# Kernel optimization log

Measured on AMD Instinct MI355X. Metric: run time of the kernel, lower is better.

The kernel has to match this reference:

```python
import jax, jax.numpy as jnp
import numpy as np

SIGMA = 0.1

def setup_inputs() -> dict:
    key = jax.random.key(0)
    k1, k2, k3 = jax.random.split(key, 3)
    B = 16384
    risk_scores = jax.random.normal(k1, (B,), dtype=jnp.float32)
    times = jax.random.uniform(k2, (B,), dtype=jnp.float32)
    events = jax.random.randint(k3, (B,), 0, 2, dtype=jnp.int32)
    return {"risk_scores": risk_scores, "times": times, "events": events}

def reference(risk_scores, times, events):
    # mask[i, j] = (times[i] < times[j]) and (events[i] == 1)
    mask = (times[:, None] < times[None, :]) & (events[:, None] == 1)  # [B, B] bool
    maskf = mask.astype(risk_scores.dtype)
    # diff[i, j] = risk_scores[j] - risk_scores[i]
    diff = risk_scores[None, :] - risk_scores[:, None]  # [B, B]
    loss = jnp.sum(jax.nn.sigmoid(diff / SIGMA) * maskf)
    count = jnp.sum(maskf)
    return loss / (count + 1e-06)
```

## Files before the change

kernel.cpp:

```cpp
#include <hip/hip_runtime.h>


#define BLOCK 256
#define RPT 4
#define ROWS_PER_TILE (BLOCK * RPT)
#define JTILE 64
#define NCOLGRP 256
#define GRID_MAIN 2048

__device__ __forceinline__ float fast_exp2(float x) { return __builtin_amdgcn_exp2f(x); }
__device__ __forceinline__ float fast_rcp(float x)  { return __builtin_amdgcn_rcpf(x); }
__device__ __forceinline__ float clamp60(float x)   { return fminf(fmaxf(x, -60.0f), 60.0f); }

__global__ __launch_bounds__(BLOCK) void k_compact(
    const float* __restrict__ r, const float* __restrict__ t,
    const int* __restrict__ ev, int B, float kscale,
    int* __restrict__ cursor,
    float2* __restrict__ sI, float2* __restrict__ sJ) {
    int g = blockIdx.x * BLOCK + threadIdx.x;
    if (g >= B) return;
    float tv = t[g];
    float s  = clamp60(r[g] * kscale);
    sJ[g] = make_float2(fast_exp2(-s), tv);
    bool pred = (ev[g] == 1);
    unsigned long long m = __ballot(pred);
    int lane = threadIdx.x & 63;
    int before = __popcll(m & ((1ull << lane) - 1ull));
    int total = __popcll(m);
    int base = 0;
    if (lane == 0 && total > 0) base = atomicAdd(cursor, total);
    base = __shfl(base, 0);
    if (pred) sI[base + before] = make_float2(fast_exp2(s), tv);
}

__global__ __launch_bounds__(BLOCK) void k_main(
    const float2* __restrict__ sI, const float2* __restrict__ sJ,
    const int* __restrict__ nactive_g,
    float* __restrict__ pL, unsigned int* __restrict__ pC) {

    const int tid = threadIdx.x;
    const int nactive = *nactive_g;
    const int nrc = (nactive + ROWS_PER_TILE - 1) / ROWS_PER_TILE;
    const int ntiles = nrc * NCOLGRP;

    __shared__ float2 tile[JTILE];

    float lsum = 0.0f;
    int   csum = 0;

    for (int tix = blockIdx.x; tix < ntiles; tix += gridDim.x) {
        int rc = tix >> 8;
        int cg = tix & (NCOLGRP - 1);

        float E[RPT], T[RPT];
        int rbase = rc * ROWS_PER_TILE;
#pragma unroll
        for (int k = 0; k < RPT; ++k) {
            int rr = rbase + tid + (k << 8);
            if (rr < nactive) { float2 f = sI[rr]; E[k] = f.x; T[k] = f.y; }
            else              { E[k] = __builtin_inff(); T[k] = 3.0f; }
        }

        __syncthreads();
        if (tid < JTILE) tile[tid] = sJ[(cg << 6) + tid];
        __syncthreads();

        float l[RPT] = {0.f, 0.f, 0.f, 0.f};
        int c = 0;
#pragma unroll 8
        for (int jj = 0; jj < JTILE; ++jj) {
            float2 q = tile[jj];
            float F = q.x, tj = q.y;
#pragma unroll
            for (int k = 0; k < RPT; ++k) {
                float sg = fast_rcp(__builtin_fmaf(E[k], F, 1.0f));
                bool m = T[k] < tj;
                l[k] += m ? sg : 0.0f;
                c += m;
            }
        }
        lsum += (l[0] + l[1]) + (l[2] + l[3]);
        csum += c;
    }

#pragma unroll
    for (int off = 32; off > 0; off >>= 1) {
        lsum += __shfl_down(lsum, off);
        csum += __shfl_down(csum, off);
    }
    __shared__ float lw[BLOCK / 64];
    __shared__ int   cw[BLOCK / 64];
    int wid = tid >> 6;
    if ((tid & 63) == 0) { lw[wid] = lsum; cw[wid] = csum; }
    __syncthreads();
    if (tid == 0) {
        pL[blockIdx.x] = (lw[0] + lw[1]) + (lw[2] + lw[3]);
        pC[blockIdx.x] = (unsigned)((cw[0] + cw[1]) + (cw[2] + cw[3]));
    }
}

__global__ __launch_bounds__(BLOCK) void k_finalize(
    const float* __restrict__ pL, const unsigned int* __restrict__ pC,
    int n, float* __restrict__ out) {
    double l = 0.0, c = 0.0;
    for (int i = threadIdx.x; i < n; i += BLOCK) {
        l += (double)pL[i];
        c += (double)pC[i];
    }
#pragma unroll
    for (int off = 32; off > 0; off >>= 1) {
        l += __shfl_down(l, off);
        c += __shfl_down(c, off);
    }
    __shared__ double lw[BLOCK / 64], cw[BLOCK / 64];
    int wid = threadIdx.x >> 6;
    if ((threadIdx.x & 63) == 0) { lw[wid] = l; cw[wid] = c; }
    __syncthreads();
    if (threadIdx.x == 0) {
        double L = (lw[0] + lw[1]) + (lw[2] + lw[3]);
        double C = (cw[0] + cw[1]) + (cw[2] + cw[3]);
        out[0] = (float)(L / (C + 1e-6));
    }
}

extern "C" void kernel_launch(void* const* d_in, const int* in_sizes, int n_in,
                              void* d_out, int out_size, void* d_ws, size_t ws_size,
                              hipStream_t stream) {
    const float* r  = (const float*)d_in[0];
    const float* t  = (const float*)d_in[1];
    const int*   ev = (const int*)d_in[2];
    float* out = (float*)d_out;
    const int B = in_sizes[0];

    const float SIGMA = 0.1f;
    const float LOG2E = 1.4426950408889634f;
    const float kscale = LOG2E / SIGMA;

    char* ws = (char*)d_ws;
    int* cursor = (int*)ws;
    float2* sI  = (float2*)(ws + 4096);
    float2* sJ  = sI + B;
    float*  pL  = (float*)(sJ + B);
    unsigned int* pC = (unsigned int*)(pL + GRID_MAIN);

    const int nblk = (B + BLOCK - 1) / BLOCK;

    hipMemsetAsync(ws, 0, 64, stream);
    k_compact<<<nblk, BLOCK, 0, stream>>>(r, t, ev, B, kscale, cursor, sI, sJ);
    k_main<<<GRID_MAIN, BLOCK, 0, stream>>>(sI, sJ, cursor, pL, pC);
    k_finalize<<<1, BLOCK, 0, stream>>>(pL, pC, GRID_MAIN, out);
}
```

Before: 42.12 us.

## Pair rows to share one reciprocal per two sigmoids and use block-level compaction

The inner loop now combines two rows' sigmoid denominators into one product, using a single reciprocal: 1/u + 1/v = (u+v)/(uv), with masked numerators selecting which terms contribute. This halves the transcendental reciprocal count per pair evaluation, which is the dominant cost of the quadratic loop. The product is clamped to avoid overflow to infinity, which could lose precision when both factors are large. The compaction kernel also issues one atomic per block instead of one per wave, at the cost of two block barriers.

```diff
diff --git a/kernel.cpp b/kernel.cpp
--- a/kernel.cpp
+++ b/kernel.cpp
@@ -17,20 +17,28 @@
     const int* __restrict__ ev, int B, float kscale,
     int* __restrict__ cursor,
     float2* __restrict__ sI, float2* __restrict__ sJ) {
-    int g = blockIdx.x * BLOCK + threadIdx.x;
+    const int tid = threadIdx.x;
+    int g = blockIdx.x * BLOCK + tid;
     if (g >= B) return;
     float tv = t[g];
     float s  = clamp60(r[g] * kscale);
     sJ[g] = make_float2(fast_exp2(-s), tv);
     bool pred = (ev[g] == 1);
-    unsigned long long m = __ballot(pred);
-    int lane = threadIdx.x & 63;
-    int before = __popcll(m & ((1ull << lane) - 1ull));
-    int total = __popcll(m);
-    int base = 0;
-    if (lane == 0 && total > 0) base = atomicAdd(cursor, total);
-    base = __shfl(base, 0);
-    if (pred) sI[base + before] = make_float2(fast_exp2(s), tv);
+    unsigned long long bal = __ballot(pred);
+    int lane = tid & 63, wid = tid >> 6;
+    int before = __popcll(bal & ((1ull << lane) - 1ull));
+    int wcnt = __popcll(bal);
+    __shared__ int wbase[BLOCK / 64];
+    if (lane == 0) wbase[wid] = wcnt;
+    __syncthreads();
+    if (tid == 0) {
+        int c0 = wbase[0], c1 = wbase[1], c2 = wbase[2], c3 = wbase[3];
+        int b0 = atomicAdd(cursor, (c0 + c1) + (c2 + c3));
+        wbase[0] = b0; wbase[1] = b0 + c0; wbase[2] = b0 + c0 + c1;
+        wbase[3] = b0 + c0 + c1 + c2;
+    }
+    __syncthreads();
+    if (pred) sI[wbase[wid] + before] = make_float2(fast_exp2(s), tv);
 }
 
 __global__ __launch_bounds__(BLOCK) void k_main(
@@ -58,28 +66,37 @@
         for (int k = 0; k < RPT; ++k) {
             int rr = rbase + tid + (k << 8);
             if (rr < nactive) { float2 f = sI[rr]; E[k] = f.x; T[k] = f.y; }
-            else              { E[k] = __builtin_inff(); T[k] = 3.0f; }
+            else              { E[k] = 1.0f; T[k] = 3.0f; }
         }
 
         __syncthreads();
         if (tid < JTILE) tile[tid] = sJ[(cg << 6) + tid];
         __syncthreads();
 
-        float l[RPT] = {0.f, 0.f, 0.f, 0.f};
+        float l0 = 0.f, l1 = 0.f;
         int c = 0;
 #pragma unroll 8
         for (int jj = 0; jj < JTILE; ++jj) {
             float2 q = tile[jj];
             float F = q.x, tj = q.y;
-#pragma unroll
-            for (int k = 0; k < RPT; ++k) {
-                float sg = fast_rcp(__builtin_fmaf(E[k], F, 1.0f));
-                bool m = T[k] < tj;
-                l[k] += m ? sg : 0.0f;
-                c += m;
-            }
+            float u0 = __builtin_fmaf(E[0], F, 1.0f);
+            float v0 = __builtin_fmaf(E[1], F, 1.0f);
+            float p0 = fminf(u0 * v0, 3.0e38f);
+            float rp0 = fast_rcp(p0);
+            bool m0 = T[0] < tj, m1 = T[1] < tj;
+            float num0 = (m0 ? v0 : 0.0f) + (m1 ? u0 : 0.0f);
+            l0 = __builtin_fmaf(num0, rp0, l0);
+            c += m0; c += m1;
+            float u1 = __builtin_fmaf(E[2], F, 1.0f);
+            float v1 = __builtin_fmaf(E[3], F, 1.0f);
+            float p1 = fminf(u1 * v1, 3.0e38f);
+            float rp1 = fast_rcp(p1);
+            bool m2 = T[2] < tj, m3 = T[3] < tj;
+            float num1 = (m2 ? v1 : 0.0f) + (m3 ? u1 : 0.0f);
+            l1 = __builtin_fmaf(num1, rp1, l1);
+            c += m2; c += m3;
         }
-        lsum += (l[0] + l[1]) + (l[2] + l[3]);
+        lsum += l0 + l1;
         csum += c;
     }
 
```

After: 42.36 us. No clear change (+0.6%).
